# Optimization experiments

Measured on AMD Instinct MI355X. Metric: run time of the kernel, lower is better.

## Reference

```python
import jax, jax.numpy as jnp
import numpy as np

B, T, C, H, K = 16, 8192, 128, 128, 5


def setup_inputs() -> dict:
    key = jax.random.key(0)
    ks = jax.random.split(key, 6)
    std = 1.0 / np.sqrt(H)  # matches reset_parameters uniform(-std, std)
    u = lambda k, s: jax.random.uniform(k, s, jnp.float32, -std, std)
    return {
        "inputs": jax.random.normal(ks[0], (B, T, C), jnp.float32),
        "init_state": jax.random.normal(ks[1], (2, B, H), jnp.float32),
        "z_w": u(ks[2], (H, C, K)),
        "z_b": u(ks[3], (H,)),
        "f_w": u(ks[4], (H, C, K)),
        "f_b": u(ks[5], (H,)),
    }


def _conv1d_same(x, w, b):
    # x: (B, C, T), w: (H, C, K) -> (B, H, T), padding='same'
    y = jax.lax.conv_general_dilated(
        x, w, window_strides=(1,), padding="SAME",
        dimension_numbers=("NCH", "OIH", "NCH"))
    return y + b[None, :, None]


def reference(inputs, init_state, z_w, z_b, f_w, f_b):
    # inputs: (B, T, C); init_state: (2, B, H)
    x = jnp.transpose(inputs, (0, 2, 1))                       # (B, C, T)
    raw_f = jnp.transpose(_conv1d_same(x, f_w, f_b), (0, 2, 1))  # (B, T, H)
    raw_z = jnp.transpose(_conv1d_same(x, z_w, z_b), (0, 2, 1))  # (B, T, H)
    # prepend init state along time -> (B, T+1, H)
    raw_f = jnp.concatenate([init_state[0][:, None, :], raw_f], axis=1)
    raw_z = jnp.concatenate([init_state[1][:, None, :], raw_z], axis=1)
    log_one_minus_f = jax.nn.log_sigmoid(-raw_f)  # mode='f'
    log_z = jax.nn.log_sigmoid(raw_z)
    log_f = jax.nn.log_sigmoid(raw_f)
    cs = jnp.cumsum(log_f, axis=1)
    # recurrent_gates[t] = log_f[t] - cumsum[t] + cumsum[-1]
    rg = log_f - cs + cs[:, -1:, :]
    log_hidden = jax.lax.cumlogsumexp(log_z + log_one_minus_f + rg, axis=1)
    return jnp.exp(log_hidden - rg)  # (B, T+1, H)
```

## Files before the change

kernel.cpp:

```cpp
#include <hip/hip_runtime.h>
#include <hip/hip_bf16.h>
#include <cstdint>

#define DEVFN __device__ __forceinline__

namespace {

constexpr int B = 16, T = 8192, C = 128, H = 128, K = 5;
constexpr int TP1 = T + 1;
constexpr int N = B * TP1 * H;
constexpr int NKK = 20;
constexpr int NCH = T / 64;
constexpr int NSER = B * H;
constexpr int WF_ELE = NKK * 8 * 64 * 2 * 8;
constexpr int XPITCH = 136;

typedef __attribute__((ext_vector_type(8))) short short8;
typedef __attribute__((ext_vector_type(4))) float f32x4;

DEVFN float sigmoidf(float x) { return 1.0f / (1.0f + __expf(-x)); }
DEVFN unsigned bfb(float v) {
  __hip_bfloat16 h = __float2bfloat16(v);
  return (unsigned)*reinterpret_cast<unsigned short*>(&h);
}

DEVFN void compose(float& P, float& Q, float& Fl, float Pr, float Qr, float Flr) {
  float t = Fl * Pr;
  P = P * t;
  Q = fmaf(t, Q, Qr);
  Fl = Flr;
}

__global__ __launch_bounds__(256)
void wprep_kernel(const float* __restrict__ fw, const float* __restrict__ zw,
                  short* __restrict__ Wfrag) {
  int idx = blockIdx.x * 256 + threadIdx.x;
  if (idx >= WF_ELE) return;
  int j = idx & 7;
  int fz = (idx >> 3) & 1;
  int lane = (idx >> 4) & 63;
  int nf8 = (idx >> 10) & 7;
  int kk = idx >> 13;
  int kdim = kk * 32 + ((lane >> 4) << 3) + j;
  int h = nf8 * 16 + (lane & 15);
  int k = kdim >> 7, c = kdim & 127;
  int src = (h * C + c) * K + k;
  float w = fz ? zw[src] : fw[src];
  Wfrag[idx] = (short)bfb(w);
}

__global__ __launch_bounds__(512, 4)
void conv_mfma_kernel(const float* __restrict__ x,
                      const float* __restrict__ fb, const float* __restrict__ zb,
                      const short* __restrict__ Wfrag,
                      unsigned* __restrict__ FG,
                      float* __restrict__ sumP, float* __restrict__ sumQ) {
  __shared__ short xs[68 * XPITCH];
  const int b = blockIdx.y;
  const int t0 = blockIdx.x * 64;
  const int tid = threadIdx.x;
  const int lane = tid & 63;
  const int wid = tid >> 6;
  const int lrow = lane & 15;
  const int lg = lane >> 4;

  for (int i = tid; i < 68 * 16; i += 512) {
    int r = i >> 4, co = (i & 15) << 3;
    int t = t0 - 2 + r;
    f32x4 v0 = {0.f, 0.f, 0.f, 0.f}, v1 = v0;
    if (t >= 0 && t < T) {
      const f32x4* p = reinterpret_cast<const f32x4*>(x + ((size_t)(b * T + t)) * C + co);
      v0 = p[0]; v1 = p[1];
    }
    short8 s;
    s[0] = (short)bfb(v0[0]); s[1] = (short)bfb(v0[1]); s[2] = (short)bfb(v0[2]); s[3] = (short)bfb(v0[3]);
    s[4] = (short)bfb(v1[0]); s[5] = (short)bfb(v1[1]); s[6] = (short)bfb(v1[2]); s[7] = (short)bfb(v1[3]);
    *reinterpret_cast<short8*>(xs + r * XPITCH + co) = s;
  }
  __syncthreads();

  f32x4 accF[4], accZ[4];
#pragma unroll
  for (int mf = 0; mf < 4; ++mf) { accF[mf] = {0.f,0.f,0.f,0.f}; accZ[mf] = {0.f,0.f,0.f,0.f}; }

  const char* xsb = reinterpret_cast<const char*>(xs);
  const short8* wb = reinterpret_cast<const short8*>(Wfrag) + (wid * 64 + lane) * 2;
  const int abase = lrow * 272 + lg * 16;

#pragma unroll
  for (int kk = 0; kk < NKK; ++kk) {
    const int k = kk >> 2;
    const int cq = (kk & 3) << 6;
    short8 bf = wb[kk * 1024];
    short8 bz = wb[kk * 1024 + 1];
    short8 a[4];
#pragma unroll
    for (int mf = 0; mf < 4; ++mf)
      a[mf] = *reinterpret_cast<const short8*>(xsb + (abase + (mf * 16 + k) * 272 + cq));
#pragma unroll
    for (int mf = 0; mf < 4; ++mf) {
      accF[mf] = __builtin_amdgcn_mfma_f32_16x16x32_bf16(a[mf], bf, accF[mf], 0, 0, 0);
      accZ[mf] = __builtin_amdgcn_mfma_f32_16x16x32_bf16(a[mf], bz, accZ[mf], 0, 0, 0);
    }
  }

  const int cblk = blockIdx.x;
  const int h = wid * 16 + lrow;
  const float biasF = fb[h], biasZ = zb[h];
  float cP = 1.f, cQ = 0.f, cFl = 1.f;
#pragma unroll
  for (int mf = 0; mf < 4; ++mf) {
    float y = 0.f, P = 1.f, prevF = 1.f;
#pragma unroll
    for (int j = 0; j < 4; ++j) {
      int m = mf * 16 + lg * 4 + j;
      int s = t0 + m + 1;
      float rf = accF[mf][j] + biasF;
      float rz = accZ[mf][j] + biasZ;
      float F = sigmoidf(rf);
      float G = sigmoidf(rz) * (1.0f - F);
      FG[(size_t)(b * TP1 + s) * H + h] = bfb(F) | (bfb(G) << 16);
      if (j == 0) { y = G; P = 1.f; }
      else { P *= prevF; y = fmaf(prevF, y, G); }
      prevF = F;
    }
    float tP = P, tQ = y, tFl = prevF;
    {
      float pP = __shfl(tP, lane + 16, 64);
      float pQ = __shfl(tQ, lane + 16, 64);
      float pF = __shfl(tFl, lane + 16, 64);
      compose(tP, tQ, tFl, pP, pQ, pF);
      pP = __shfl(tP, lane + 32, 64);
      pQ = __shfl(tQ, lane + 32, 64);
      pF = __shfl(tFl, lane + 32, 64);
      compose(tP, tQ, tFl, pP, pQ, pF);
    }
    if (mf == 0) { cP = tP; cQ = tQ; cFl = tFl; }
    else compose(cP, cQ, cFl, tP, tQ, tFl);
  }
  if (lg == 0) {
    int sidx = cblk * NSER + b * H + h;
    sumP[sidx] = cP;
    sumQ[sidx] = cQ;
  }
}

__global__ void scanB_kernel(const float* __restrict__ init,
                             const unsigned* __restrict__ FG_r,
                             unsigned* __restrict__ FG_w,
                             const float* __restrict__ sumQ,
                             float* __restrict__ sumP_cin,
                             float* __restrict__ out) {
  int g = blockIdx.x * blockDim.x + threadIdx.x;
  int b = g >> 7, h = g & (H - 1);
  float rf = init[g];
  float rz = init[NSER + g];
  float F0 = sigmoidf(rf), z = sigmoidf(rz);
  float G0 = z * (1.0f - F0);
  size_t base = (size_t)b * TP1 * H + h;
  FG_w[base] = bfb(F0) | (bfb(G0) << 16);
  out[base] = G0;
  float y = G0;
  float prevFl = F0;
  for (int j = 0; j < NCH; ++j) {
    int sidx = j * NSER + g;
    float Ps = sumP_cin[sidx];
    float Q  = sumQ[sidx];
    sumP_cin[sidx] = y;
    y = fmaf(prevFl * Ps, y, Q);
    if (j + 1 < NCH)
      prevFl = __uint_as_float(FG_r[base + (size_t)(64 * (j + 1)) * H] << 16);
  }
}

__global__ __launch_bounds__(128)
void scanC_kernel(const unsigned* __restrict__ FG, const float* __restrict__ cin,
                  float* __restrict__ out) {
  const int b = blockIdx.y, j = blockIdx.x, h = threadIdx.x;
  const int s0 = 1 + j * 64;
  float y = cin[j * NSER + b * H + h];
  const size_t base = (size_t)b * TP1 * H + h;
  const unsigned* p = FG + base + (size_t)s0 * H;
  float Fprev = __uint_as_float(p[-H] << 16);
  float* po = out + base + (size_t)s0 * H;
#pragma unroll 8
  for (int t = 0; t < 64; ++t) {
    unsigned u = *p; p += H;
    float G = __uint_as_float(u & 0xffff0000u);
    y = fmaf(Fprev, y, G);
    Fprev = __uint_as_float(u << 16);
    *po = y; po += H;
  }
}

}

extern "C" void kernel_launch(void* const* d_in, const int* in_sizes, int n_in,
                              void* d_out, int out_size, void* d_ws, size_t ws_size,
                              hipStream_t stream) {
  const float* x    = (const float*)d_in[0];
  const float* init = (const float*)d_in[1];
  const float* zw   = (const float*)d_in[2];
  const float* zb   = (const float*)d_in[3];
  const float* fw   = (const float*)d_in[4];
  const float* fb   = (const float*)d_in[5];
  float* out = (float*)d_out;
  char* ws = (char*)d_ws;

  unsigned* FG = (unsigned*)ws;
  float* sumP = (float*)(ws + (size_t)N * 4);
  float* sumQ = sumP + (size_t)NCH * NSER;
  short* Wfrag = (short*)(sumQ + (size_t)NCH * NSER);

  wprep_kernel<<<(WF_ELE + 255) / 256, 256, 0, stream>>>(fw, zw, Wfrag);
  conv_mfma_kernel<<<dim3(NCH, B), 512, 0, stream>>>(x, fb, zb, Wfrag, FG, sumP, sumQ);
  scanB_kernel<<<16, 128, 0, stream>>>(init, FG, FG, sumQ, sumP, out);
  scanC_kernel<<<dim3(NCH, B), 128, 0, stream>>>(FG, sumP, out);
}
```

Before: 109.1 us.

## Halve conv block to 4 waves, each computing two H-fragments with prefetched weights

The conv kernel now launches 256 threads per block, and each wave computes two 16-wide H fragments instead of one. Each A fragment loaded from LDS is therefore reused across twice as many MFMAs, cutting LDS traffic per FLOP. Weight fragments for the next kk step are prefetched into registers while the current step's MFMAs run. In exchange, accumulator and weight register use roughly doubles, which can lower occupancy, and each block has half as many waves to load x and hide latency.

```diff
diff --git a/kernel.cpp b/kernel.cpp
--- a/kernel.cpp
+++ b/kernel.cpp
@@ -49,7 +49,7 @@
   Wfrag[idx] = (short)bfb(w);
 }
 
-__global__ __launch_bounds__(512, 4)
+__global__ __launch_bounds__(256, 4)
 void conv_mfma_kernel(const float* __restrict__ x,
                       const float* __restrict__ fb, const float* __restrict__ zb,
                       const short* __restrict__ Wfrag,
@@ -64,7 +64,7 @@
   const int lrow = lane & 15;
   const int lg = lane >> 4;
 
-  for (int i = tid; i < 68 * 16; i += 512) {
+  for (int i = tid; i < 68 * 16; i += 256) {
     int r = i >> 4, co = (i & 15) << 3;
     int t = t0 - 2 + r;
     f32x4 v0 = {0.f, 0.f, 0.f, 0.f}, v1 = v0;
@@ -79,70 +79,83 @@
   }
   __syncthreads();
 
-  f32x4 accF[4], accZ[4];
-#pragma unroll
-  for (int mf = 0; mf < 4; ++mf) { accF[mf] = {0.f,0.f,0.f,0.f}; accZ[mf] = {0.f,0.f,0.f,0.f}; }
+  f32x4 accF0[4], accZ0[4], accF1[4], accZ1[4];
+#pragma unroll
+  for (int mf = 0; mf < 4; ++mf) {
+    accF0[mf] = {0.f,0.f,0.f,0.f}; accZ0[mf] = {0.f,0.f,0.f,0.f};
+    accF1[mf] = {0.f,0.f,0.f,0.f}; accZ1[mf] = {0.f,0.f,0.f,0.f};
+  }
 
   const char* xsb = reinterpret_cast<const char*>(xs);
-  const short8* wb = reinterpret_cast<const short8*>(Wfrag) + (wid * 64 + lane) * 2;
+  const short8* wb = reinterpret_cast<const short8*>(Wfrag) + (wid * 256 + lane * 2);
   const int abase = lrow * 272 + lg * 16;
 
+  short8 wf0 = wb[0], wz0 = wb[1], wf1 = wb[128], wz1 = wb[129];
+
 #pragma unroll
   for (int kk = 0; kk < NKK; ++kk) {
+    short8 cf0 = wf0, cz0 = wz0, cf1 = wf1, cz1 = wz1;
+    if (kk + 1 < NKK) {
+      const int o = (kk + 1) * 1024;
+      wf0 = wb[o]; wz0 = wb[o + 1]; wf1 = wb[o + 128]; wz1 = wb[o + 129];
+    }
     const int k = kk >> 2;
     const int cq = (kk & 3) << 6;
-    short8 bf = wb[kk * 1024];
-    short8 bz = wb[kk * 1024 + 1];
     short8 a[4];
 #pragma unroll
     for (int mf = 0; mf < 4; ++mf)
       a[mf] = *reinterpret_cast<const short8*>(xsb + (abase + (mf * 16 + k) * 272 + cq));
 #pragma unroll
     for (int mf = 0; mf < 4; ++mf) {
-      accF[mf] = __builtin_amdgcn_mfma_f32_16x16x32_bf16(a[mf], bf, accF[mf], 0, 0, 0);
-      accZ[mf] = __builtin_amdgcn_mfma_f32_16x16x32_bf16(a[mf], bz, accZ[mf], 0, 0, 0);
+      accF0[mf] = __builtin_amdgcn_mfma_f32_16x16x32_bf16(a[mf], cf0, accF0[mf], 0, 0, 0);
+      accZ0[mf] = __builtin_amdgcn_mfma_f32_16x16x32_bf16(a[mf], cz0, accZ0[mf], 0, 0, 0);
+      accF1[mf] = __builtin_amdgcn_mfma_f32_16x16x32_bf16(a[mf], cf1, accF1[mf], 0, 0, 0);
+      accZ1[mf] = __builtin_amdgcn_mfma_f32_16x16x32_bf16(a[mf], cz1, accZ1[mf], 0, 0, 0);
     }
   }
 
   const int cblk = blockIdx.x;
-  const int h = wid * 16 + lrow;
-  const float biasF = fb[h], biasZ = zb[h];
-  float cP = 1.f, cQ = 0.f, cFl = 1.f;
-#pragma unroll
-  for (int mf = 0; mf < 4; ++mf) {
-    float y = 0.f, P = 1.f, prevF = 1.f;
-#pragma unroll
-    for (int j = 0; j < 4; ++j) {
-      int m = mf * 16 + lg * 4 + j;
-      int s = t0 + m + 1;
-      float rf = accF[mf][j] + biasF;
-      float rz = accZ[mf][j] + biasZ;
-      float F = sigmoidf(rf);
-      float G = sigmoidf(rz) * (1.0f - F);
-      FG[(size_t)(b * TP1 + s) * H + h] = bfb(F) | (bfb(G) << 16);
-      if (j == 0) { y = G; P = 1.f; }
-      else { P *= prevF; y = fmaf(prevF, y, G); }
-      prevF = F;
-    }
-    float tP = P, tQ = y, tFl = prevF;
-    {
-      float pP = __shfl(tP, lane + 16, 64);
-      float pQ = __shfl(tQ, lane + 16, 64);
-      float pF = __shfl(tFl, lane + 16, 64);
-      compose(tP, tQ, tFl, pP, pQ, pF);
-      pP = __shfl(tP, lane + 32, 64);
-      pQ = __shfl(tQ, lane + 32, 64);
-      pF = __shfl(tFl, lane + 32, 64);
-      compose(tP, tQ, tFl, pP, pQ, pF);
-    }
-    if (mf == 0) { cP = tP; cQ = tQ; cFl = tFl; }
-    else compose(cP, cQ, cFl, tP, tQ, tFl);
-  }
-  if (lg == 0) {
-    int sidx = cblk * NSER + b * H + h;
-    sumP[sidx] = cP;
-    sumQ[sidx] = cQ;
-  }
+  auto epilogue = [&](const f32x4* aF, const f32x4* aZ, int h) {
+    const float biasF = fb[h], biasZ = zb[h];
+    float cP = 1.f, cQ = 0.f, cFl = 1.f;
+#pragma unroll
+    for (int mf = 0; mf < 4; ++mf) {
+      float y = 0.f, P = 1.f, prevF = 1.f;
+#pragma unroll
+      for (int j = 0; j < 4; ++j) {
+        int m = mf * 16 + lg * 4 + j;
+        int s = t0 + m + 1;
+        float rf = aF[mf][j] + biasF;
+        float rz = aZ[mf][j] + biasZ;
+        float F = sigmoidf(rf);
+        float G = sigmoidf(rz) * (1.0f - F);
+        FG[(size_t)(b * TP1 + s) * H + h] = bfb(F) | (bfb(G) << 16);
+        if (j == 0) { y = G; P = 1.f; }
+        else { P *= prevF; y = fmaf(prevF, y, G); }
+        prevF = F;
+      }
+      float tP = P, tQ = y, tFl = prevF;
+      {
+        float pP = __shfl(tP, lane + 16, 64);
+        float pQ = __shfl(tQ, lane + 16, 64);
+        float pF = __shfl(tFl, lane + 16, 64);
+        compose(tP, tQ, tFl, pP, pQ, pF);
+        pP = __shfl(tP, lane + 32, 64);
+        pQ = __shfl(tQ, lane + 32, 64);
+        pF = __shfl(tFl, lane + 32, 64);
+        compose(tP, tQ, tFl, pP, pQ, pF);
+      }
+      if (mf == 0) { cP = tP; cQ = tQ; cFl = tFl; }
+      else compose(cP, cQ, cFl, tP, tQ, tFl);
+    }
+    if (lg == 0) {
+      int sidx = cblk * NSER + b * H + h;
+      sumP[sidx] = cP;
+      sumQ[sidx] = cQ;
+    }
+  };
+  epilogue(accF0, accZ0, wid * 32 + lrow);
+  epilogue(accF1, accZ1, wid * 32 + 16 + lrow);
 }
 
 __global__ void scanB_kernel(const float* __restrict__ init,
@@ -213,7 +226,7 @@
   short* Wfrag = (short*)(sumQ + (size_t)NCH * NSER);
 
   wprep_kernel<<<(WF_ELE + 255) / 256, 256, 0, stream>>>(fw, zw, Wfrag);
-  conv_mfma_kernel<<<dim3(NCH, B), 512, 0, stream>>>(x, fb, zb, Wfrag, FG, sumP, sumQ);
+  conv_mfma_kernel<<<dim3(NCH, B), 256, 0, stream>>>(x, fb, zb, Wfrag, FG, sumP, sumQ);
   scanB_kernel<<<16, 128, 0, stream>>>(init, FG, FG, sumQ, sumP, out);
   scanC_kernel<<<dim3(NCH, B), 128, 0, stream>>>(FG, sumP, out);
 }
```

Result: no change. 107.7 us (-1.3%).

## Enlarge conv tile to 128 timesteps with 2x4 wave grid per block

Applied to the files above, without the earlier changes.

The conv kernel tile grows from 64 to 128 time rows. Its 8 waves are arranged as 2 row-groups by 4 column-groups, and each wave computes 32 output channels instead of 16. The halo overhead per block shrinks and each A fragment loaded from LDS is reused across four MFMAs, so there are fewer blocks and less redundant x loading. The cost is twice the accumulator registers per wave, which may lower occupancy under the 512x4 launch bound.

```diff
diff --git a/kernel.cpp b/kernel.cpp
--- a/kernel.cpp
+++ b/kernel.cpp
@@ -14,6 +14,8 @@
 constexpr int NSER = B * H;
 constexpr int WF_ELE = NKK * 8 * 64 * 2 * 8;
 constexpr int XPITCH = 136;
+constexpr int BM = 128;
+constexpr int XROWS = BM + 4;
 
 typedef __attribute__((ext_vector_type(8))) short short8;
 typedef __attribute__((ext_vector_type(4))) float f32x4;
@@ -55,16 +57,18 @@
                       const short* __restrict__ Wfrag,
                       unsigned* __restrict__ FG,
                       float* __restrict__ sumP, float* __restrict__ sumQ) {
-  __shared__ short xs[68 * XPITCH];
+  __shared__ short xs[XROWS * XPITCH];
   const int b = blockIdx.y;
-  const int t0 = blockIdx.x * 64;
+  const int t0 = blockIdx.x * BM;
   const int tid = threadIdx.x;
   const int lane = tid & 63;
   const int wid = tid >> 6;
+  const int wm = wid >> 2;
+  const int wn = wid & 3;
   const int lrow = lane & 15;
   const int lg = lane >> 4;
 
-  for (int i = tid; i < 68 * 16; i += 512) {
+  for (int i = tid; i < XROWS * 16; i += 512) {
     int r = i >> 4, co = (i & 15) << 3;
     int t = t0 - 2 + r;
     f32x4 v0 = {0.f, 0.f, 0.f, 0.f}, v1 = v0;
@@ -79,69 +83,83 @@
   }
   __syncthreads();
 
-  f32x4 accF[4], accZ[4];
-#pragma unroll
-  for (int mf = 0; mf < 4; ++mf) { accF[mf] = {0.f,0.f,0.f,0.f}; accZ[mf] = {0.f,0.f,0.f,0.f}; }
+  f32x4 accF0[4], accZ0[4], accF1[4], accZ1[4];
+#pragma unroll
+  for (int mf = 0; mf < 4; ++mf) {
+    accF0[mf] = {0.f,0.f,0.f,0.f}; accZ0[mf] = {0.f,0.f,0.f,0.f};
+    accF1[mf] = {0.f,0.f,0.f,0.f}; accZ1[mf] = {0.f,0.f,0.f,0.f};
+  }
 
   const char* xsb = reinterpret_cast<const char*>(xs);
-  const short8* wb = reinterpret_cast<const short8*>(Wfrag) + (wid * 64 + lane) * 2;
-  const int abase = lrow * 272 + lg * 16;
+  const short8* wb = reinterpret_cast<const short8*>(Wfrag) + (wn * 256 + lane * 2);
+  const int abase = (wm * 64 + lrow) * 272 + lg * 16;
 
 #pragma unroll
   for (int kk = 0; kk < NKK; ++kk) {
     const int k = kk >> 2;
     const int cq = (kk & 3) << 6;
-    short8 bf = wb[kk * 1024];
-    short8 bz = wb[kk * 1024 + 1];
+    const int o = kk * 1024;
+    short8 f0 = wb[o], z0 = wb[o + 1], f1 = wb[o + 128], z1 = wb[o + 129];
     short8 a[4];
 #pragma unroll
     for (int mf = 0; mf < 4; ++mf)
       a[mf] = *reinterpret_cast<const short8*>(xsb + (abase + (mf * 16 + k) * 272 + cq));
 #pragma unroll
     for (int mf = 0; mf < 4; ++mf) {
-      accF[mf] = __builtin_amdgcn_mfma_f32_16x16x32_bf16(a[mf], bf, accF[mf], 0, 0, 0);
-      accZ[mf] = __builtin_amdgcn_mfma_f32_16x16x32_bf16(a[mf], bz, accZ[mf], 0, 0, 0);
-    }
-  }
-
-  const int cblk = blockIdx.x;
-  const int h = wid * 16 + lrow;
-  const float biasF = fb[h], biasZ = zb[h];
-  float cP = 1.f, cQ = 0.f, cFl = 1.f;
+      accF0[mf] = __builtin_amdgcn_mfma_f32_16x16x32_bf16(a[mf], f0, accF0[mf], 0, 0, 0);
+      accZ0[mf] = __builtin_amdgcn_mfma_f32_16x16x32_bf16(a[mf], z0, accZ0[mf], 0, 0, 0);
+      accF1[mf] = __builtin_amdgcn_mfma_f32_16x16x32_bf16(a[mf], f1, accF1[mf], 0, 0, 0);
+      accZ1[mf] = __builtin_amdgcn_mfma_f32_16x16x32_bf16(a[mf], z1, accZ1[mf], 0, 0, 0);
+    }
+  }
+
+  const int h0 = wn * 32 + lrow, h1 = h0 + 16;
+  const float bF0 = fb[h0], bZ0 = zb[h0], bF1 = fb[h1], bZ1 = zb[h1];
+  float cP0 = 1.f, cQ0 = 0.f, cFl0 = 1.f;
+  float cP1 = 1.f, cQ1 = 0.f, cFl1 = 1.f;
 #pragma unroll
   for (int mf = 0; mf < 4; ++mf) {
-    float y = 0.f, P = 1.f, prevF = 1.f;
+    float y0 = 0.f, P0 = 1.f, pF0 = 1.f;
+    float y1 = 0.f, P1 = 1.f, pF1 = 1.f;
 #pragma unroll
     for (int j = 0; j < 4; ++j) {
       int m = mf * 16 + lg * 4 + j;
-      int s = t0 + m + 1;
-      float rf = accF[mf][j] + biasF;
-      float rz = accZ[mf][j] + biasZ;
-      float F = sigmoidf(rf);
-      float G = sigmoidf(rz) * (1.0f - F);
-      FG[(size_t)(b * TP1 + s) * H + h] = bfb(F) | (bfb(G) << 16);
-      if (j == 0) { y = G; P = 1.f; }
-      else { P *= prevF; y = fmaf(prevF, y, G); }
-      prevF = F;
-    }
-    float tP = P, tQ = y, tFl = prevF;
+      int s = t0 + wm * 64 + m + 1;
+      size_t off = (size_t)(b * TP1 + s) * H;
+      float F0 = sigmoidf(accF0[mf][j] + bF0);
+      float G0 = sigmoidf(accZ0[mf][j] + bZ0) * (1.0f - F0);
+      float F1 = sigmoidf(accF1[mf][j] + bF1);
+      float G1 = sigmoidf(accZ1[mf][j] + bZ1) * (1.0f - F1);
+      FG[off + h0] = bfb(F0) | (bfb(G0) << 16);
+      FG[off + h1] = bfb(F1) | (bfb(G1) << 16);
+      if (j == 0) { y0 = G0; y1 = G1; }
+      else {
+        P0 *= pF0; y0 = fmaf(pF0, y0, G0);
+        P1 *= pF1; y1 = fmaf(pF1, y1, G1);
+      }
+      pF0 = F0; pF1 = F1;
+    }
+    float tP0 = P0, tQ0 = y0, tF0 = pF0;
+    float tP1 = P1, tQ1 = y1, tF1 = pF1;
     {
-      float pP = __shfl(tP, lane + 16, 64);
-      float pQ = __shfl(tQ, lane + 16, 64);
-      float pF = __shfl(tFl, lane + 16, 64);
-      compose(tP, tQ, tFl, pP, pQ, pF);
-      pP = __shfl(tP, lane + 32, 64);
-      pQ = __shfl(tQ, lane + 32, 64);
-      pF = __shfl(tFl, lane + 32, 64);
-      compose(tP, tQ, tFl, pP, pQ, pF);
-    }
-    if (mf == 0) { cP = tP; cQ = tQ; cFl = tFl; }
-    else compose(cP, cQ, cFl, tP, tQ, tFl);
+      float q;
+      q = __shfl(tP0, lane + 16, 64); float r0 = __shfl(tQ0, lane + 16, 64); float s0 = __shfl(tF0, lane + 16, 64);
+      compose(tP0, tQ0, tF0, q, r0, s0);
+      q = __shfl(tP1, lane + 16, 64); float r1 = __shfl(tQ1, lane + 16, 64); float s1 = __shfl(tF1, lane + 16, 64);
+      compose(tP1, tQ1, tF1, q, r1, s1);
+      q = __shfl(tP0, lane + 32, 64); r0 = __shfl(tQ0, lane + 32, 64); s0 = __shfl(tF0, lane + 32, 64);
+      compose(tP0, tQ0, tF0, q, r0, s0);
+      q = __shfl(tP1, lane + 32, 64); r1 = __shfl(tQ1, lane + 32, 64); s1 = __shfl(tF1, lane + 32, 64);
+      compose(tP1, tQ1, tF1, q, r1, s1);
+    }
+    if (mf == 0) { cP0 = tP0; cQ0 = tQ0; cFl0 = tF0; cP1 = tP1; cQ1 = tQ1; cFl1 = tF1; }
+    else { compose(cP0, cQ0, cFl0, tP0, tQ0, tF0); compose(cP1, cQ1, cFl1, tP1, tQ1, tF1); }
   }
   if (lg == 0) {
-    int sidx = cblk * NSER + b * H + h;
-    sumP[sidx] = cP;
-    sumQ[sidx] = cQ;
+    int cix = blockIdx.x * 2 + wm;
+    int sbase = cix * NSER + b * H;
+    sumP[sbase + h0] = cP0; sumQ[sbase + h0] = cQ0;
+    sumP[sbase + h1] = cP1; sumQ[sbase + h1] = cQ1;
   }
 }
 
@@ -213,7 +231,7 @@
   short* Wfrag = (short*)(sumQ + (size_t)NCH * NSER);
 
   wprep_kernel<<<(WF_ELE + 255) / 256, 256, 0, stream>>>(fw, zw, Wfrag);
-  conv_mfma_kernel<<<dim3(NCH, B), 512, 0, stream>>>(x, fb, zb, Wfrag, FG, sumP, sumQ);
+  conv_mfma_kernel<<<dim3(NCH / 2, B), 512, 0, stream>>>(x, fb, zb, Wfrag, FG, sumP, sumQ);
   scanB_kernel<<<16, 128, 0, stream>>>(init, FG, FG, sumQ, sumP, out);
   scanC_kernel<<<dim3(NCH, B), 128, 0, stream>>>(FG, sumP, out);
 }
```

Measured after the change: 108.0 us. No clear change (-1.0%).
